# Performance work log

Hardware: AMD Instinct MI355X
Metric: run time of the kernel (lower is better)

The kernel has to match this reference:

```python
import jax, jax.numpy as jnp
import numpy as np

N, NS, IN_P, OUT_P, SHARE = 65536, 16, 256, 256, 8
MID = OUT_P
EPS = 1e-5


def _bn(x, gamma, beta):
    # torch BatchNorm1d (training mode, biased var) applied over the channel
    # (last) axis; stats over all other axes. Matches BN on x.transpose(1,2).
    mean = x.mean(axis=(0, 1), keepdims=True)
    var = ((x - mean) ** 2).mean(axis=(0, 1), keepdims=True)
    return gamma * (x - mean) * jax.lax.rsqrt(var + EPS) + beta


def setup_inputs() -> dict:
    key = jax.random.key(0)
    ks = jax.random.split(key, 12)
    w = lambda k, shape: jax.random.normal(k, shape, dtype=jnp.float32) * 0.02
    return {
        "p": jax.random.uniform(ks[0], (N, 3), dtype=jnp.float32),
        "x": jax.random.normal(ks[1], (N, IN_P), dtype=jnp.float32),
        "idx": jax.random.randint(ks[2], (N, NS), 0, N),
        "wq": w(ks[3], (MID, IN_P)), "bq": jnp.zeros((MID,), jnp.float32),
        "wk": w(ks[4], (MID, IN_P)), "bk": jnp.zeros((MID,), jnp.float32),
        "wv": w(ks[5], (OUT_P, IN_P)), "bv": jnp.zeros((OUT_P,), jnp.float32),
        "wp1": w(ks[6], (3, 3)), "bp1": jnp.zeros((3,), jnp.float32),
        "gp": jnp.ones((3,), jnp.float32), "btp": jnp.zeros((3,), jnp.float32),
        "wp2": w(ks[7], (OUT_P, 3)), "bp2": jnp.zeros((OUT_P,), jnp.float32),
        "g1": jnp.ones((MID,), jnp.float32), "b1": jnp.zeros((MID,), jnp.float32),
        "ww1": w(ks[8], (MID // SHARE, MID)), "bw1": jnp.zeros((MID // SHARE,), jnp.float32),
        "g2": jnp.ones((MID // SHARE,), jnp.float32), "b2": jnp.zeros((MID // SHARE,), jnp.float32),
        "ww2": w(ks[9], (OUT_P // SHARE, OUT_P // SHARE)), "bw2": jnp.zeros((OUT_P // SHARE,), jnp.float32),
    }


def reference(p, x, idx, wq, bq, wk, bk, wv, bv, wp1, bp1, gp, btp, wp2, bp2,
              g1, b1, ww1, bw1, g2, b2, ww2, bw2):
    # q/k/v projections: [N, C]
    xq = x @ wq.T + bq
    xk = x @ wk.T + bk
    xv = x @ wv.T + bv
    # queryandgroup: gather neighbor features + relative positions
    xk_g = xk[idx]                      # [N, NS, MID]
    xv_g = xv[idx]                      # [N, NS, OUT_P]
    p_r = p[idx] - p[:, None, :]        # [N, NS, 3]  (use_xyz relative coords)
    # linear_p: Linear(3,3) -> BN(3) -> ReLU -> Linear(3, OUT_P)
    p_r = p_r @ wp1.T + bp1
    p_r = jax.nn.relu(_bn(p_r, gp, btp))
    p_r = p_r @ wp2.T + bp2             # [N, NS, OUT_P]
    # vector attention logits; out_planes // mid_planes == 1 so the
    # view(...).sum(2) of p_r is just p_r
    w = xk_g - xq[:, None, :] + p_r     # [N, NS, MID]
    # linear_w: BN -> ReLU -> Linear(MID, MID/S) -> BN -> ReLU -> Linear
    w = jax.nn.relu(_bn(w, g1, b1))
    w = w @ ww1.T + bw1                 # [N, NS, MID/S]
    w = jax.nn.relu(_bn(w, g2, b2))
    w = w @ ww2.T + bw2                 # [N, NS, OUT_P/S]
    w = jax.nn.softmax(w, axis=1)       # softmax over neighbors
    # grouped weighted sum with shared attention planes
    n, ns, c = xv_g.shape
    out = ((xv_g + p_r).reshape(n, ns, SHARE, c // SHARE)
           * w[:, :, None, :]).sum(axis=1).reshape(n, c)
    return out
```

## Files before the change

kernel.cpp:

```cpp
#include <hip/hip_runtime.h>
#include <hip/hip_bf16.h>

#define NPTS 65536
#define NSAMP 16
#define CH 256
#define CNT (NPTS * NSAMP)
#define EPSV 1e-5f

typedef __hip_bfloat16 bf16;
typedef __attribute__((ext_vector_type(8))) short short8;
typedef __attribute__((ext_vector_type(4))) short sh4;
typedef __attribute__((ext_vector_type(4))) float floatx4;

__device__ __forceinline__ float b2f(bf16 v) { return __bfloat162float(v); }

__device__ __forceinline__ float s2f(short v) {
    return __uint_as_float(((unsigned)(unsigned short)v) << 16);
}

__device__ __forceinline__ short f2bf_bits(float f) {
    bf16 h = __float2bfloat16(f);
    short s;
    __builtin_memcpy(&s, &h, 2);
    return s;
}

__global__ __launch_bounds__(256) void convw_kernel(
    const float* __restrict__ wq, const float* __restrict__ wk,
    const float* __restrict__ wv, const float* __restrict__ ww2,
    const float* __restrict__ x,
    bf16* __restrict__ Wcat, bf16* __restrict__ ww2b, bf16* __restrict__ xb)
{
    if (blockIdx.x < 96) {
        int e = (blockIdx.x * 256 + threadIdx.x) * 8;
        const float* src = (e < 65536) ? wq : (e < 131072) ? wk : wv;
        int off = e & 65535;
        float4 f0 = *(const float4*)(src + off);
        float4 f1 = *(const float4*)(src + off + 4);
        short8 r;
        r[0] = f2bf_bits(f0.x); r[1] = f2bf_bits(f0.y);
        r[2] = f2bf_bits(f0.z); r[3] = f2bf_bits(f0.w);
        r[4] = f2bf_bits(f1.x); r[5] = f2bf_bits(f1.y);
        r[6] = f2bf_bits(f1.z); r[7] = f2bf_bits(f1.w);
        *(short8*)(Wcat + e) = r;
    } else if (blockIdx.x == 96) {
        int e = threadIdx.x * 4;
        float4 f = *(const float4*)(ww2 + e);
        sh4 r;
        r[0] = f2bf_bits(f.x); r[1] = f2bf_bits(f.y);
        r[2] = f2bf_bits(f.z); r[3] = f2bf_bits(f.w);
        *(sh4*)(ww2b + e) = r;
    } else {
        size_t e = ((size_t)(blockIdx.x - 97) * 256 + threadIdx.x) * 8;
        float4 f0 = *(const float4*)(x + e);
        float4 f1 = *(const float4*)(x + e + 4);
        short8 r;
        r[0] = f2bf_bits(f0.x); r[1] = f2bf_bits(f0.y);
        r[2] = f2bf_bits(f0.z); r[3] = f2bf_bits(f0.w);
        r[4] = f2bf_bits(f1.x); r[5] = f2bf_bits(f1.y);
        r[6] = f2bf_bits(f1.z); r[7] = f2bf_bits(f1.w);
        *(short8*)(xb + e) = r;
    }
}

__global__ __launch_bounds__(256) void gemm_kernel(
    const bf16* __restrict__ xb, const bf16* __restrict__ Wcat,
    const float* __restrict__ bq, const float* __restrict__ bk,
    const float* __restrict__ bv,
    bf16* __restrict__ xq, bf16* __restrict__ xk, bf16* __restrict__ xv)
{
    __shared__ __align__(16) bf16 As[128 * 40];
    __shared__ __align__(16) bf16 Bs[128 * 40];

    int t = threadIdx.x, lane = t & 63, wave = t >> 6;
    int m0 = blockIdx.x * 128;
    int y = blockIdx.y, n0 = y * 128;
    int srow = t >> 1, sch = t & 1;
    int m = lane & 15, q = lane >> 4;
    int wm = wave >> 1, wn = wave & 1;

    floatx4 acc[4][4];
#pragma unroll
    for (int a = 0; a < 4; a++)
#pragma unroll
        for (int b = 0; b < 4; b++) acc[a][b] = (floatx4){0.f, 0.f, 0.f, 0.f};

    for (int kk = 0; kk < 256; kk += 32) {
        const bf16* ap = xb + (size_t)(m0 + srow) * 256 + kk + sch * 16;
        *(short8*)&As[srow * 40 + sch * 16]     = *(const short8*)ap;
        *(short8*)&As[srow * 40 + sch * 16 + 8] = *(const short8*)(ap + 8);
        const bf16* bp = Wcat + (size_t)(n0 + srow) * 256 + kk + sch * 16;
        *(short8*)&Bs[srow * 40 + sch * 16]     = *(const short8*)bp;
        *(short8*)&Bs[srow * 40 + sch * 16 + 8] = *(const short8*)(bp + 8);
        __syncthreads();

        short8 av[4], bvv[4];
#pragma unroll
        for (int mt = 0; mt < 4; mt++)
            av[mt] = *(const short8*)&As[(wm * 64 + mt * 16 + m) * 40 + q * 8];
#pragma unroll
        for (int nt = 0; nt < 4; nt++)
            bvv[nt] = *(const short8*)&Bs[(wn * 64 + nt * 16 + m) * 40 + q * 8];
#pragma unroll
        for (int mt = 0; mt < 4; mt++)
#pragma unroll
            for (int nt = 0; nt < 4; nt++)
                acc[mt][nt] = __builtin_amdgcn_mfma_f32_16x16x32_bf16(av[mt], bvv[nt], acc[mt][nt], 0, 0, 0);
        __syncthreads();
    }

    int z = y >> 1;
    bf16* O        = (z == 0) ? xq : (z == 1) ? xk : xv;
    const float* B = (z == 0) ? bq : (z == 1) ? bk : bv;
    int cbase = (y & 1) * 128 + wn * 64;
#pragma unroll
    for (int nt = 0; nt < 4; nt++) {
        int oc = cbase + nt * 16 + m;
        float bias = B[oc];
#pragma unroll
        for (int mt = 0; mt < 4; mt++) {
            int grow = m0 + wm * 64 + mt * 16 + q * 4;
#pragma unroll
            for (int i = 0; i < 4; i++)
                O[(size_t)(grow + i) * 256 + oc] = __float2bfloat16(acc[mt][nt][i] + bias);
        }
    }
}

__global__ __launch_bounds__(256) void statsp_kernel(
    const float* __restrict__ p, const int* __restrict__ idx,
    const float* __restrict__ wp1, const float* __restrict__ bp1,
    float* __restrict__ statsP, float4* __restrict__ v4)
{
    __shared__ float red[4][6];

    float W00 = wp1[0], W01 = wp1[1], W02 = wp1[2];
    float W10 = wp1[3], W11 = wp1[4], W12 = wp1[5];
    float W20 = wp1[6], W21 = wp1[7], W22 = wp1[8];
    float B0 = bp1[0], B1 = bp1[1], B2 = bp1[2];

    float s0 = 0, s1 = 0, s2 = 0, q0 = 0, q1 = 0, q2 = 0;
    int stride = gridDim.x * blockDim.x;
    for (int r = blockIdx.x * blockDim.x + threadIdx.x; r < CNT; r += stride) {
        int n = r >> 4;
        int i = idx[r];
        float a0 = p[3 * (size_t)i]     - p[3 * (size_t)n];
        float a1 = p[3 * (size_t)i + 1] - p[3 * (size_t)n + 1];
        float a2 = p[3 * (size_t)i + 2] - p[3 * (size_t)n + 2];
        float v0 = W00 * a0 + W01 * a1 + W02 * a2 + B0;
        float v1 = W10 * a0 + W11 * a1 + W12 * a2 + B1;
        float v2 = W20 * a0 + W21 * a1 + W22 * a2 + B2;
        s0 += v0; q0 += v0 * v0;
        s1 += v1; q1 += v1 * v1;
        s2 += v2; q2 += v2 * v2;
        v4[r] = make_float4(v0, v1, v2, 0.f);
    }
    float v[6] = {s0, s1, s2, q0, q1, q2};
    int wave = threadIdx.x >> 6;
#pragma unroll
    for (int k = 0; k < 6; k++) {
        float xv = v[k];
#pragma unroll
        for (int off = 32; off > 0; off >>= 1) xv += __shfl_down(xv, off);
        if ((threadIdx.x & 63) == 0) red[wave][k] = xv;
    }
    __syncthreads();
    if (threadIdx.x < 6) {
        float s = red[0][threadIdx.x] + red[1][threadIdx.x]
                + red[2][threadIdx.x] + red[3][threadIdx.x];
        atomicAdd(&statsP[threadIdx.x * 16], s);
    }
}

__global__ void finalize_kernel(const float* __restrict__ stats,
                                const float* __restrict__ gamma,
                                const float* __restrict__ beta,
                                float* __restrict__ ss, int nch, int sstr)
{
    int c = threadIdx.x;
    if (c < nch) {
        float inv = 1.0f / (float)CNT;
        float mean = stats[c * sstr] * inv;
        float var = stats[(nch + c) * sstr] * inv - mean * mean;
        float sc = gamma[c] * rsqrtf(var + EPSV);
        ss[c] = sc;
        ss[nch + c] = beta[c] - mean * sc;
    }
}

__global__ __launch_bounds__(256) void computer_kernel(
    const float* __restrict__ ssP, float4* __restrict__ r4)
{
    float sc0 = ssP[0], sc1 = ssP[1], sc2 = ssP[2];
    float sh0 = ssP[3], sh1 = ssP[4], sh2 = ssP[5];

    int stride = gridDim.x * blockDim.x;
    for (int r = blockIdx.x * blockDim.x + threadIdx.x; r < CNT; r += stride) {
        float4 v = r4[r];
        float v0 = fmaxf(sc0 * v.x + sh0, 0.f);
        float v1 = fmaxf(sc1 * v.y + sh1, 0.f);
        float v2 = fmaxf(sc2 * v.z + sh2, 0.f);
        r4[r] = make_float4(v0, v1, v2, 0.f);
    }
}

__global__ __launch_bounds__(256) void stats1_kernel(
    const int* __restrict__ idx, const float4* __restrict__ r4,
    const bf16* __restrict__ xk, const bf16* __restrict__ xq,
    const float* __restrict__ wp2, const float* __restrict__ bp2,
    float* __restrict__ stats1)
{
    __shared__ int idxs[1024];
    __shared__ float redS[8 * 264];
    __shared__ float redQ[8 * 264];

    int t = threadIdx.x;
    int r0 = blockIdx.x * 1024;
    for (int e = t; e < 1024; e += 256) idxs[e] = idx[r0 + e];

    int sub = t & 31, rl = t >> 5, cb = sub * 8;
    float w0[8], w1[8], w2[8], bc[8];
#pragma unroll
    for (int k = 0; k < 8; k++) {
        w0[k] = wp2[3 * (cb + k)];
        w1[k] = wp2[3 * (cb + k) + 1];
        w2[k] = wp2[3 * (cb + k) + 2];
        bc[k] = bp2[cb + k];
    }
    float s8[8] = {0, 0, 0, 0, 0, 0, 0, 0};
    float q8[8] = {0, 0, 0, 0, 0, 0, 0, 0};
    __syncthreads();

#pragma unroll 4
    for (int rr = rl; rr < 1024; rr += 8) {
        int r = r0 + rr;
        int i = idxs[rr];
        float4 rv = r4[r];
        short8 kv = *(const short8*)(xk + (size_t)i * 256 + cb);
        short8 qv = *(const short8*)(xq + (size_t)(r >> 4) * 256 + cb);
#pragma unroll
        for (int k = 0; k < 8; k++) {
            float w = s2f(kv[k]) - s2f(qv[k]) + rv.x * w0[k] + rv.y * w1[k] + rv.z * w2[k] + bc[k];
            s8[k] += w; q8[k] += w * w;
        }
    }
#pragma unroll
    for (int k = 0; k < 8; k++) {
        redS[rl * 264 + cb + k] = s8[k];
        redQ[rl * 264 + cb + k] = q8[k];
    }
    __syncthreads();
    int c = t;
    float ts = 0, tq = 0;
#pragma unroll
    for (int sr = 0; sr < 8; sr++) {
        ts += redS[sr * 264 + c];
        tq += redQ[sr * 264 + c];
    }
    atomicAdd(&stats1[c], ts);
    atomicAdd(&stats1[256 + c], tq);
}

__global__ __launch_bounds__(256) void stats2_kernel(
    const int* __restrict__ idx, const float4* __restrict__ r4,
    const bf16* __restrict__ xk, const bf16* __restrict__ xq,
    const float* __restrict__ wp2, const float* __restrict__ bp2,
    const float* __restrict__ ss1,
    const float* __restrict__ ww1, const float* __restrict__ bw1,
    bf16* __restrict__ y2, float* __restrict__ stats2)
{
    __shared__ __align__(16) bf16 hb0[64 * 256];
    __shared__ __align__(16) bf16 hb1[64 * 256];

    int t = threadIdx.x;
    int lane = t & 63, wave = t >> 6;
    int m = lane & 15, q = lane >> 4;
    int sub = t & 31, rl = t >> 5, cb = sub * 8;
    int r0 = blockIdx.x * 1024;

    short8 bf0[8], bf1[8];
#pragma unroll
    for (int k = 0; k < 8; k++) {
        const float* w0p = ww1 + m * 256 + k * 32 + q * 8;
        const float* w1p = ww1 + (16 + m) * 256 + k * 32 + q * 8;
        float4 u0 = *(const float4*)(w0p);
        float4 u1 = *(const float4*)(w0p + 4);
        float4 u2 = *(const float4*)(w1p);
        float4 u3 = *(const float4*)(w1p + 4);
        short8 b0, b1;
        b0[0] = f2bf_bits(u0.x); b0[1] = f2bf_bits(u0.y);
        b0[2] = f2bf_bits(u0.z); b0[3] = f2bf_bits(u0.w);
        b0[4] = f2bf_bits(u1.x); b0[5] = f2bf_bits(u1.y);
        b0[6] = f2bf_bits(u1.z); b0[7] = f2bf_bits(u1.w);
        b1[0] = f2bf_bits(u2.x); b1[1] = f2bf_bits(u2.y);
        b1[2] = f2bf_bits(u2.z); b1[3] = f2bf_bits(u2.w);
        b1[4] = f2bf_bits(u3.x); b1[5] = f2bf_bits(u3.y);
        b1[6] = f2bf_bits(u3.z); b1[7] = f2bf_bits(u3.w);
        bf0[k] = b0; bf1[k] = b1;
    }

    float w0[8], w1[8], w2[8], bc[8], s1c[8], t1c[8];
#pragma unroll
    for (int k = 0; k < 8; k++) {
        w0[k] = wp2[3 * (cb + k)];
        w1[k] = wp2[3 * (cb + k) + 1];
        w2[k] = wp2[3 * (cb + k) + 2];
        bc[k] = bp2[cb + k];
        s1c[k] = ss1[cb + k];
        t1c[k] = ss1[256 + cb + k];
    }
    float bw0 = bw1[m], bw16 = bw1[16 + m];
    float jsum0 = 0, jsum1 = 0, jsq0 = 0, jsq1 = 0;
    int swh = cb ^ (rl << 3);
    int swa = (m & 7) << 3;

    {
#pragma unroll
        for (int u = 0; u < 8; u++) {
            int rr = rl + u * 8;
            int r = r0 + rr;
            int i = idx[r];
            float4 rv = r4[r];
            short8 kv = *(const short8*)(xk + (size_t)i * 256 + cb);
            short8 qv = *(const short8*)(xq + (size_t)(r >> 4) * 256 + cb);
            short8 h;
#pragma unroll
            for (int k = 0; k < 8; k++) {
                float w = s2f(kv[k]) - s2f(qv[k]) + rv.x * w0[k] + rv.y * w1[k] + rv.z * w2[k] + bc[k];
                h[k] = f2bf_bits(fmaxf(s1c[k] * w + t1c[k], 0.f));
            }
            *(short8*)&hb0[rr * 256 + swh] = h;
        }
    }

    for (int it = 0; it < 16; ++it) {
        __syncthreads();

        int rbn = r0 + (it + 1) * 64;
        bf16* hbw = (it & 1) ? hb0 : hb1;
        const bf16* abase = ((it & 1) ? hb1 : hb0) + (wave * 16 + m) * 256;

        short8 kvs[8];
        if (it < 15) {
#pragma unroll
            for (int u = 0; u < 8; u++) {
                int r = rbn + rl + u * 8;
                kvs[u] = *(const short8*)(xk + (size_t)idx[r] * 256 + cb);
            }
        }

        floatx4 a0 = (floatx4){bw0, bw0, bw0, bw0};
        floatx4 a1 = (floatx4){bw16, bw16, bw16, bw16};
#pragma unroll
        for (int k = 0; k < 8; k++) {
            int col = (k * 32 + q * 8) ^ swa;
            short8 af = *(const short8*)(abase + col);
            a0 = __builtin_amdgcn_mfma_f32_16x16x32_bf16(af, bf0[k], a0, 0, 0, 0);
            a1 = __builtin_amdgcn_mfma_f32_16x16x32_bf16(af, bf1[k], a1, 0, 0, 0);
        }
        int grow = r0 + it * 64 + wave * 16 + q * 4;
#pragma unroll
        for (int ii = 0; ii < 4; ii++) {
            float y0 = a0[ii];
            float y1 = a1[ii];
            jsum0 += y0; jsq0 += y0 * y0;
            jsum1 += y1; jsq1 += y1 * y1;
            y2[(size_t)(grow + ii) * 32 + m]      = __float2bfloat16(y0);
            y2[(size_t)(grow + ii) * 32 + 16 + m] = __float2bfloat16(y1);
        }

        if (it < 15) {
#pragma unroll
            for (int u = 0; u < 8; u++) {
                int rr = rl + u * 8;
                int r = rbn + rr;
                float4 rv = r4[r];
                short8 qv = *(const short8*)(xq + (size_t)(r >> 4) * 256 + cb);
                short8 h;
#pragma unroll
                for (int k = 0; k < 8; k++) {
                    float w = s2f(kvs[u][k]) - s2f(qv[k]) + rv.x * w0[k] + rv.y * w1[k] + rv.z * w2[k] + bc[k];
                    h[k] = f2bf_bits(fmaxf(s1c[k] * w + t1c[k], 0.f));
                }
                *(short8*)&hbw[rr * 256 + swh] = h;
            }
        }
    }

    jsum0 += __shfl_xor(jsum0, 16); jsum0 += __shfl_xor(jsum0, 32);
    jsum1 += __shfl_xor(jsum1, 16); jsum1 += __shfl_xor(jsum1, 32);
    jsq0  += __shfl_xor(jsq0, 16);  jsq0  += __shfl_xor(jsq0, 32);
    jsq1  += __shfl_xor(jsq1, 16);  jsq1  += __shfl_xor(jsq1, 32);
    if (q == 0) {
        atomicAdd(&stats2[m], jsum0);
        atomicAdd(&stats2[16 + m], jsum1);
        atomicAdd(&stats2[32 + m], jsq0);
        atomicAdd(&stats2[48 + m], jsq1);
    }
}

__global__ __launch_bounds__(256) void final_kernel(
    const int* __restrict__ idx, const float4* __restrict__ r4,
    const bf16* __restrict__ xv,
    const float* __restrict__ wp2, const float* __restrict__ bp2,
    const bf16* __restrict__ y2, const float* __restrict__ ss2,
    const bf16* __restrict__ ww2b, const float* __restrict__ bw2,
    float* __restrict__ out)
{
    __shared__ __align__(16) float wsm[4][16][36];
    __shared__ float Asm[4][4][32];

    int t = threadIdx.x, wave = t >> 6, lane = t & 63;
    int m = lane & 15, q = lane >> 4;

    short8 bf0 = *(const short8*)(ww2b + m * 32 + q * 8);
    short8 bf1 = *(const short8*)(ww2b + (16 + m) * 32 + q * 8);
    float bwj0 = bw2[m], bwj1 = bw2[16 + m];

    float s2c[8], t2c[8];
#pragma unroll
    for (int k = 0; k < 8; k++) {
        s2c[k] = ss2[q * 8 + k];
        t2c[k] = ss2[32 + q * 8 + k];
    }

    int c0 = lane * 4;
    int j4 = (lane & 7) * 4;
    float wpc0[4], wpc1[4], wpc2[4], bpc[4];
#pragma unroll
    for (int k = 0; k < 4; k++) {
        wpc0[k] = wp2[(c0 + k) * 3];
        wpc1[k] = wp2[(c0 + k) * 3 + 1];
        wpc2[k] = wp2[(c0 + k) * 3 + 2];
        bpc[k]  = bp2[c0 + k];
    }

    int pbase = (blockIdx.x * 4 + wave) * 8;
    for (int pp = 0; pp < 8; pp++) {
        int n = pbase + pp;
        size_t rbase = (size_t)n * 16;

        int iv = idx[rbase + m];

        short8 yv = *(const short8*)(y2 + (rbase + m) * 32 + q * 8);
        short8 av;
#pragma unroll
        for (int k = 0; k < 8; k++)
            av[k] = f2bf_bits(fmaxf(s2c[k] * s2f(yv[k]) + t2c[k], 0.f));

        floatx4 l0 = (floatx4){bwj0, bwj0, bwj0, bwj0};
        floatx4 l1 = (floatx4){bwj1, bwj1, bwj1, bwj1};
        l0 = __builtin_amdgcn_mfma_f32_16x16x32_bf16(av, bf0, l0, 0, 0, 0);
        l1 = __builtin_amdgcn_mfma_f32_16x16x32_bf16(av, bf1, l1, 0, 0, 0);

        float mx0 = fmaxf(fmaxf(l0[0], l0[1]), fmaxf(l0[2], l0[3]));
        float mx1 = fmaxf(fmaxf(l1[0], l1[1]), fmaxf(l1[2], l1[3]));
        mx0 = fmaxf(mx0, __shfl_xor(mx0, 16));
        mx0 = fmaxf(mx0, __shfl_xor(mx0, 32));
        mx1 = fmaxf(mx1, __shfl_xor(mx1, 16));
        mx1 = fmaxf(mx1, __shfl_xor(mx1, 32));
        float w0[4], w1[4];
        float sum0 = 0.f, sum1 = 0.f;
#pragma unroll
        for (int i = 0; i < 4; i++) {
            w0[i] = __expf(l0[i] - mx0); sum0 += w0[i];
            w1[i] = __expf(l1[i] - mx1); sum1 += w1[i];
        }
        sum0 += __shfl_xor(sum0, 16); sum0 += __shfl_xor(sum0, 32);
        sum1 += __shfl_xor(sum1, 16); sum1 += __shfl_xor(sum1, 32);
        float inv0 = 1.f / sum0, inv1 = 1.f / sum1;

        float A00 = 0, A10 = 0, A20 = 0, A30 = 0;
        float A01 = 0, A11 = 0, A21 = 0, A31 = 0;
#pragma unroll
        for (int i = 0; i < 4; i++) {
            w0[i] *= inv0; w1[i] *= inv1;
            float4 rv = r4[rbase + q * 4 + i];
            A00 += rv.x * w0[i]; A10 += rv.y * w0[i];
            A20 += rv.z * w0[i]; A30 += w0[i];
            A01 += rv.x * w1[i]; A11 += rv.y * w1[i];
            A21 += rv.z * w1[i]; A31 += w1[i];
            wsm[wave][q * 4 + i][m]      = w0[i];
            wsm[wave][q * 4 + i][16 + m] = w1[i];
        }
        A00 += __shfl_xor(A00, 16); A00 += __shfl_xor(A00, 32);
        A10 += __shfl_xor(A10, 16); A10 += __shfl_xor(A10, 32);
        A20 += __shfl_xor(A20, 16); A20 += __shfl_xor(A20, 32);
        A30 += __shfl_xor(A30, 16); A30 += __shfl_xor(A30, 32);
        A01 += __shfl_xor(A01, 16); A01 += __shfl_xor(A01, 32);
        A11 += __shfl_xor(A11, 16); A11 += __shfl_xor(A11, 32);
        A21 += __shfl_xor(A21, 16); A21 += __shfl_xor(A21, 32);
        A31 += __shfl_xor(A31, 16); A31 += __shfl_xor(A31, 32);
        if (q == 0) {
            Asm[wave][0][m] = A00; Asm[wave][1][m] = A10;
            Asm[wave][2][m] = A20; Asm[wave][3][m] = A30;
            Asm[wave][0][16 + m] = A01; Asm[wave][1][16 + m] = A11;
            Asm[wave][2][16 + m] = A21; Asm[wave][3][16 + m] = A31;
        }

        float acc0 = 0, acc1 = 0, acc2 = 0, acc3 = 0;
#pragma unroll
        for (int s = 0; s < 16; s++) {
            int i = __builtin_amdgcn_readlane(iv, s);
            sh4 vv = *(const sh4*)(xv + (size_t)i * 256 + c0);
            float4 wv = *(const float4*)&wsm[wave][s][j4];
            acc0 += s2f(vv[0]) * wv.x;
            acc1 += s2f(vv[1]) * wv.y;
            acc2 += s2f(vv[2]) * wv.z;
            acc3 += s2f(vv[3]) * wv.w;
        }

        float res[4] = {acc0, acc1, acc2, acc3};
#pragma unroll
        for (int k = 0; k < 4; k++) {
            int j = j4 + k;
            res[k] += wpc0[k] * Asm[wave][0][j] + wpc1[k] * Asm[wave][1][j]
                    + wpc2[k] * Asm[wave][2][j] + bpc[k]  * Asm[wave][3][j];
        }
        *(float4*)(out + (size_t)n * 256 + c0) =
            make_float4(res[0], res[1], res[2], res[3]);
    }
}

extern "C" void kernel_launch(void* const* d_in, const int* in_sizes, int n_in,
                              void* d_out, int out_size, void* d_ws, size_t ws_size,
                              hipStream_t stream) {
    (void)in_sizes; (void)n_in; (void)out_size; (void)ws_size;

    const float* p   = (const float*)d_in[0];
    const float* x   = (const float*)d_in[1];
    const int*   idx = (const int*)d_in[2];
    const float* wq  = (const float*)d_in[3];  const float* bq  = (const float*)d_in[4];
    const float* wk  = (const float*)d_in[5];  const float* bk  = (const float*)d_in[6];
    const float* wv  = (const float*)d_in[7];  const float* bv  = (const float*)d_in[8];
    const float* wp1 = (const float*)d_in[9];  const float* bp1 = (const float*)d_in[10];
    const float* gp  = (const float*)d_in[11]; const float* btp = (const float*)d_in[12];
    const float* wp2 = (const float*)d_in[13]; const float* bp2 = (const float*)d_in[14];
    const float* g1  = (const float*)d_in[15]; const float* b1  = (const float*)d_in[16];
    const float* ww1 = (const float*)d_in[17]; const float* bw1 = (const float*)d_in[18];
    const float* g2  = (const float*)d_in[19]; const float* b2  = (const float*)d_in[20];
    const float* ww2 = (const float*)d_in[21]; const float* bw2 = (const float*)d_in[22];
    float* out = (float*)d_out;

    float* fws    = (float*)d_ws;
    float* statsP = fws;
    float* ssP    = fws + 96;
    float* stats1 = fws + 112;
    float* ss1    = fws + 624;
    float* stats2 = fws + 1136;
    float* ss2    = fws + 1200;
    bf16* ww2b = (bf16*)((char*)d_ws + 6144);
    bf16* Wcat = (bf16*)((char*)d_ws + 8192);
    bf16* xq = (bf16*)((char*)d_ws + 401408);
    bf16* xk = xq + (size_t)NPTS * CH;
    bf16* xv = xk + (size_t)NPTS * CH;
    bf16* y2 = xv + (size_t)NPTS * CH;
    float4* r4 = (float4*)(y2 + (size_t)CNT * 32);
    bf16* xb = y2;

    hipMemsetAsync(d_ws, 0, 8192, stream);

    convw_kernel<<<97 + 8192, 256, 0, stream>>>(wq, wk, wv, ww2, x, Wcat, ww2b, xb);
    gemm_kernel<<<dim3(512, 6), 256, 0, stream>>>(xb, Wcat, bq, bk, bv, xq, xk, xv);
    statsp_kernel<<<1024, 256, 0, stream>>>(p, idx, wp1, bp1, statsP, r4);
    finalize_kernel<<<1, 256, 0, stream>>>(statsP, gp, btp, ssP, 3, 16);
    computer_kernel<<<1024, 256, 0, stream>>>(ssP, r4);
    stats1_kernel<<<1024, 256, 0, stream>>>(idx, r4, xk, xq, wp2, bp2, stats1);
    finalize_kernel<<<1, 256, 0, stream>>>(stats1, g1, b1, ss1, 256, 1);
    stats2_kernel<<<1024, 256, 0, stream>>>(idx, r4, xk, xq, wp2, bp2, ss1, ww1, bw1, y2, stats2);
    finalize_kernel<<<1, 256, 0, stream>>>(stats2, g2, b2, ss2, 32, 1);
    final_kernel<<<NPTS / 32, 256, 0, stream>>>(idx, r4, xv, wp2, bp2, y2, ss2, ww2b, bw2, out);
}
```

Before: 663.6 us.

## Fuse position-stats into conversion kernel, apply BN-ReLU on load, widen stats2 blocks

The position BN statistics pass now runs inside the weight/x conversion kernel as extra blocks, which saves one launch and lets the two passes overlap. The separate pass that rewrote r4 with BN+ReLU is removed; each consumer kernel applies the scale/shift and ReLU when it loads r4. This drops a full read-write sweep over a 16 MB buffer at the price of a little repeated ALU work. stats2 now uses 512-thread blocks with 8 waves split into 4 row-groups × 2 column halves, so each wave issues one MFMA chain instead of two and fewer gathers per thread. That trades per-wave register use for more parallelism.

```diff
diff --git a/kernel.cpp b/kernel.cpp
--- a/kernel.cpp
+++ b/kernel.cpp
@@ -25,14 +25,56 @@
     return s;
 }
 
-__global__ __launch_bounds__(256) void convw_kernel(
+__global__ __launch_bounds__(256) void fused0_kernel(
     const float* __restrict__ wq, const float* __restrict__ wk,
     const float* __restrict__ wv, const float* __restrict__ ww2,
-    const float* __restrict__ x,
-    bf16* __restrict__ Wcat, bf16* __restrict__ ww2b, bf16* __restrict__ xb)
+    const float* __restrict__ x, const float* __restrict__ p,
+    const int* __restrict__ idx,
+    const float* __restrict__ wp1, const float* __restrict__ bp1,
+    bf16* __restrict__ Wcat, bf16* __restrict__ ww2b, bf16* __restrict__ xb,
+    float* __restrict__ statsP, float4* __restrict__ v4)
 {
-    if (blockIdx.x < 96) {
-        int e = (blockIdx.x * 256 + threadIdx.x) * 8;
+    __shared__ float red[4][6];
+    int bid = blockIdx.x;
+
+    if (bid < 1024) {
+        float W00 = wp1[0], W01 = wp1[1], W02 = wp1[2];
+        float W10 = wp1[3], W11 = wp1[4], W12 = wp1[5];
+        float W20 = wp1[6], W21 = wp1[7], W22 = wp1[8];
+        float B0 = bp1[0], B1 = bp1[1], B2 = bp1[2];
+
+        float s0 = 0, s1 = 0, s2 = 0, q0 = 0, q1 = 0, q2 = 0;
+        for (int r = bid * 256 + threadIdx.x; r < CNT; r += 1024 * 256) {
+            int n = r >> 4;
+            int i = idx[r];
+            float a0 = p[3 * (size_t)i]     - p[3 * (size_t)n];
+            float a1 = p[3 * (size_t)i + 1] - p[3 * (size_t)n + 1];
+            float a2 = p[3 * (size_t)i + 2] - p[3 * (size_t)n + 2];
+            float v0 = W00 * a0 + W01 * a1 + W02 * a2 + B0;
+            float v1 = W10 * a0 + W11 * a1 + W12 * a2 + B1;
+            float v2 = W20 * a0 + W21 * a1 + W22 * a2 + B2;
+            s0 += v0; q0 += v0 * v0;
+            s1 += v1; q1 += v1 * v1;
+            s2 += v2; q2 += v2 * v2;
+            v4[r] = make_float4(v0, v1, v2, 0.f);
+        }
+        float v[6] = {s0, s1, s2, q0, q1, q2};
+        int wave = threadIdx.x >> 6;
+#pragma unroll
+        for (int k = 0; k < 6; k++) {
+            float xv = v[k];
+#pragma unroll
+            for (int off = 32; off > 0; off >>= 1) xv += __shfl_down(xv, off);
+            if ((threadIdx.x & 63) == 0) red[wave][k] = xv;
+        }
+        __syncthreads();
+        if (threadIdx.x < 6) {
+            float s = red[0][threadIdx.x] + red[1][threadIdx.x]
+                    + red[2][threadIdx.x] + red[3][threadIdx.x];
+            atomicAdd(&statsP[threadIdx.x * 16], s);
+        }
+    } else if (bid < 1120) {
+        int e = ((bid - 1024) * 256 + threadIdx.x) * 8;
         const float* src = (e < 65536) ? wq : (e < 131072) ? wk : wv;
         int off = e & 65535;
         float4 f0 = *(const float4*)(src + off);
@@ -43,7 +85,7 @@
         r[4] = f2bf_bits(f1.x); r[5] = f2bf_bits(f1.y);
         r[6] = f2bf_bits(f1.z); r[7] = f2bf_bits(f1.w);
         *(short8*)(Wcat + e) = r;
-    } else if (blockIdx.x == 96) {
+    } else if (bid == 1120) {
         int e = threadIdx.x * 4;
         float4 f = *(const float4*)(ww2 + e);
         sh4 r;
@@ -51,7 +93,7 @@
         r[2] = f2bf_bits(f.z); r[3] = f2bf_bits(f.w);
         *(sh4*)(ww2b + e) = r;
     } else {
-        size_t e = ((size_t)(blockIdx.x - 97) * 256 + threadIdx.x) * 8;
+        size_t e = ((size_t)(bid - 1121) * 256 + threadIdx.x) * 8;
         float4 f0 = *(const float4*)(x + e);
         float4 f1 = *(const float4*)(x + e + 4);
         short8 r;
@@ -124,51 +166,6 @@
             for (int i = 0; i < 4; i++)
                 O[(size_t)(grow + i) * 256 + oc] = __float2bfloat16(acc[mt][nt][i] + bias);
         }
-    }
-}
-
-__global__ __launch_bounds__(256) void statsp_kernel(
-    const float* __restrict__ p, const int* __restrict__ idx,
-    const float* __restrict__ wp1, const float* __restrict__ bp1,
-    float* __restrict__ statsP, float4* __restrict__ v4)
-{
-    __shared__ float red[4][6];
-
-    float W00 = wp1[0], W01 = wp1[1], W02 = wp1[2];
-    float W10 = wp1[3], W11 = wp1[4], W12 = wp1[5];
-    float W20 = wp1[6], W21 = wp1[7], W22 = wp1[8];
-    float B0 = bp1[0], B1 = bp1[1], B2 = bp1[2];
-
-    float s0 = 0, s1 = 0, s2 = 0, q0 = 0, q1 = 0, q2 = 0;
-    int stride = gridDim.x * blockDim.x;
-    for (int r = blockIdx.x * blockDim.x + threadIdx.x; r < CNT; r += stride) {
-        int n = r >> 4;
-        int i = idx[r];
-        float a0 = p[3 * (size_t)i]     - p[3 * (size_t)n];
-        float a1 = p[3 * (size_t)i + 1] - p[3 * (size_t)n + 1];
-        float a2 = p[3 * (size_t)i + 2] - p[3 * (size_t)n + 2];
-        float v0 = W00 * a0 + W01 * a1 + W02 * a2 + B0;
-        float v1 = W10 * a0 + W11 * a1 + W12 * a2 + B1;
-        float v2 = W20 * a0 + W21 * a1 + W22 * a2 + B2;
-        s0 += v0; q0 += v0 * v0;
-        s1 += v1; q1 += v1 * v1;
-        s2 += v2; q2 += v2 * v2;
-        v4[r] = make_float4(v0, v1, v2, 0.f);
-    }
-    float v[6] = {s0, s1, s2, q0, q1, q2};
-    int wave = threadIdx.x >> 6;
-#pragma unroll
-    for (int k = 0; k < 6; k++) {
-        float xv = v[k];
-#pragma unroll
-        for (int off = 32; off > 0; off >>= 1) xv += __shfl_down(xv, off);
-        if ((threadIdx.x & 63) == 0) red[wave][k] = xv;
-    }
-    __syncthreads();
-    if (threadIdx.x < 6) {
-        float s = red[0][threadIdx.x] + red[1][threadIdx.x]
-                + red[2][threadIdx.x] + red[3][threadIdx.x];
-        atomicAdd(&statsP[threadIdx.x * 16], s);
     }
 }
 
@@ -188,27 +185,11 @@
     }
 }
 
-__global__ __launch_bounds__(256) void computer_kernel(
-    const float* __restrict__ ssP, float4* __restrict__ r4)
-{
-    float sc0 = ssP[0], sc1 = ssP[1], sc2 = ssP[2];
-    float sh0 = ssP[3], sh1 = ssP[4], sh2 = ssP[5];
-
-    int stride = gridDim.x * blockDim.x;
-    for (int r = blockIdx.x * blockDim.x + threadIdx.x; r < CNT; r += stride) {
-        float4 v = r4[r];
-        float v0 = fmaxf(sc0 * v.x + sh0, 0.f);
-        float v1 = fmaxf(sc1 * v.y + sh1, 0.f);
-        float v2 = fmaxf(sc2 * v.z + sh2, 0.f);
-        r4[r] = make_float4(v0, v1, v2, 0.f);
-    }
-}
-
 __global__ __launch_bounds__(256) void stats1_kernel(
     const int* __restrict__ idx, const float4* __restrict__ r4,
     const bf16* __restrict__ xk, const bf16* __restrict__ xq,
     const float* __restrict__ wp2, const float* __restrict__ bp2,
-    float* __restrict__ stats1)
+    const float* __restrict__ ssP, float* __restrict__ stats1)
 {
     __shared__ int idxs[1024];
     __shared__ float redS[8 * 264];
@@ -227,6 +208,8 @@
         w2[k] = wp2[3 * (cb + k) + 2];
         bc[k] = bp2[cb + k];
     }
+    float scP0 = ssP[0], scP1 = ssP[1], scP2 = ssP[2];
+    float shP0 = ssP[3], shP1 = ssP[4], shP2 = ssP[5];
     float s8[8] = {0, 0, 0, 0, 0, 0, 0, 0};
     float q8[8] = {0, 0, 0, 0, 0, 0, 0, 0};
     __syncthreads();
@@ -235,12 +218,15 @@
     for (int rr = rl; rr < 1024; rr += 8) {
         int r = r0 + rr;
         int i = idxs[rr];
-        float4 rv = r4[r];
+        float4 va = r4[r];
+        float rx = fmaxf(scP0 * va.x + shP0, 0.f);
+        float ry = fmaxf(scP1 * va.y + shP1, 0.f);
+        float rz = fmaxf(scP2 * va.z + shP2, 0.f);
         short8 kv = *(const short8*)(xk + (size_t)i * 256 + cb);
         short8 qv = *(const short8*)(xq + (size_t)(r >> 4) * 256 + cb);
 #pragma unroll
         for (int k = 0; k < 8; k++) {
-            float w = s2f(kv[k]) - s2f(qv[k]) + rv.x * w0[k] + rv.y * w1[k] + rv.z * w2[k] + bc[k];
+            float w = s2f(kv[k]) - s2f(qv[k]) + rx * w0[k] + ry * w1[k] + rz * w2[k] + bc[k];
             s8[k] += w; q8[k] += w * w;
         }
     }
@@ -261,11 +247,11 @@
     atomicAdd(&stats1[256 + c], tq);
 }
 
-__global__ __launch_bounds__(256) void stats2_kernel(
+__global__ __launch_bounds__(512, 4) void stats2_kernel(
     const int* __restrict__ idx, const float4* __restrict__ r4,
     const bf16* __restrict__ xk, const bf16* __restrict__ xq,
     const float* __restrict__ wp2, const float* __restrict__ bp2,
-    const float* __restrict__ ss1,
+    const float* __restrict__ ssP, const float* __restrict__ ss1,
     const float* __restrict__ ww1, const float* __restrict__ bw1,
     bf16* __restrict__ y2, float* __restrict__ stats2)
 {
@@ -275,28 +261,22 @@
     int t = threadIdx.x;
     int lane = t & 63, wave = t >> 6;
     int m = lane & 15, q = lane >> 4;
+    int wr = wave >> 1, wc = wave & 1;
     int sub = t & 31, rl = t >> 5, cb = sub * 8;
     int r0 = blockIdx.x * 1024;
 
-    short8 bf0[8], bf1[8];
+    short8 bf[8];
 #pragma unroll
     for (int k = 0; k < 8; k++) {
-        const float* w0p = ww1 + m * 256 + k * 32 + q * 8;
-        const float* w1p = ww1 + (16 + m) * 256 + k * 32 + q * 8;
-        float4 u0 = *(const float4*)(w0p);
-        float4 u1 = *(const float4*)(w0p + 4);
-        float4 u2 = *(const float4*)(w1p);
-        float4 u3 = *(const float4*)(w1p + 4);
-        short8 b0, b1;
-        b0[0] = f2bf_bits(u0.x); b0[1] = f2bf_bits(u0.y);
-        b0[2] = f2bf_bits(u0.z); b0[3] = f2bf_bits(u0.w);
-        b0[4] = f2bf_bits(u1.x); b0[5] = f2bf_bits(u1.y);
-        b0[6] = f2bf_bits(u1.z); b0[7] = f2bf_bits(u1.w);
-        b1[0] = f2bf_bits(u2.x); b1[1] = f2bf_bits(u2.y);
-        b1[2] = f2bf_bits(u2.z); b1[3] = f2bf_bits(u2.w);
-        b1[4] = f2bf_bits(u3.x); b1[5] = f2bf_bits(u3.y);
-        b1[6] = f2bf_bits(u3.z); b1[7] = f2bf_bits(u3.w);
-        bf0[k] = b0; bf1[k] = b1;
+        const float* wp = ww1 + (wc * 16 + m) * 256 + k * 32 + q * 8;
+        float4 u0 = *(const float4*)(wp);
+        float4 u1 = *(const float4*)(wp + 4);
+        short8 b;
+        b[0] = f2bf_bits(u0.x); b[1] = f2bf_bits(u0.y);
+        b[2] = f2bf_bits(u0.z); b[3] = f2bf_bits(u0.w);
+        b[4] = f2bf_bits(u1.x); b[5] = f2bf_bits(u1.y);
+        b[6] = f2bf_bits(u1.z); b[7] = f2bf_bits(u1.w);
+        bf[k] = b;
     }
 
     float w0[8], w1[8], w2[8], bc[8], s1c[8], t1c[8];
@@ -309,28 +289,31 @@
         s1c[k] = ss1[cb + k];
         t1c[k] = ss1[256 + cb + k];
     }
-    float bw0 = bw1[m], bw16 = bw1[16 + m];
-    float jsum0 = 0, jsum1 = 0, jsq0 = 0, jsq1 = 0;
-    int swh = cb ^ (rl << 3);
+    float scP0 = ssP[0], scP1 = ssP[1], scP2 = ssP[2];
+    float shP0 = ssP[3], shP1 = ssP[4], shP2 = ssP[5];
+    float bwv = bw1[wc * 16 + m];
+    float jsum = 0, jsq = 0;
+    int swh = cb ^ ((rl & 7) << 3);
     int swa = (m & 7) << 3;
 
-    {
-#pragma unroll
-        for (int u = 0; u < 8; u++) {
-            int rr = rl + u * 8;
-            int r = r0 + rr;
-            int i = idx[r];
-            float4 rv = r4[r];
-            short8 kv = *(const short8*)(xk + (size_t)i * 256 + cb);
-            short8 qv = *(const short8*)(xq + (size_t)(r >> 4) * 256 + cb);
-            short8 h;
-#pragma unroll
-            for (int k = 0; k < 8; k++) {
-                float w = s2f(kv[k]) - s2f(qv[k]) + rv.x * w0[k] + rv.y * w1[k] + rv.z * w2[k] + bc[k];
-                h[k] = f2bf_bits(fmaxf(s1c[k] * w + t1c[k], 0.f));
-            }
-            *(short8*)&hb0[rr * 256 + swh] = h;
-        }
+#pragma unroll
+    for (int u = 0; u < 4; u++) {
+        int rr = rl + u * 16;
+        int r = r0 + rr;
+        int i = idx[r];
+        float4 va = r4[r];
+        float rx = fmaxf(scP0 * va.x + shP0, 0.f);
+        float ry = fmaxf(scP1 * va.y + shP1, 0.f);
+        float rz = fmaxf(scP2 * va.z + shP2, 0.f);
+        short8 kv = *(const short8*)(xk + (size_t)i * 256 + cb);
+        short8 qv = *(const short8*)(xq + (size_t)(r >> 4) * 256 + cb);
+        short8 h;
+#pragma unroll
+        for (int k = 0; k < 8; k++) {
+            float w = s2f(kv[k]) - s2f(qv[k]) + rx * w0[k] + ry * w1[k] + rz * w2[k] + bc[k];
+            h[k] = f2bf_bits(fmaxf(s1c[k] * w + t1c[k], 0.f));
+        }
+        *(short8*)&hb0[rr * 256 + swh] = h;
     }
 
     for (int it = 0; it < 16; ++it) {
@@ -338,48 +321,46 @@
 
         int rbn = r0 + (it + 1) * 64;
         bf16* hbw = (it & 1) ? hb0 : hb1;
-        const bf16* abase = ((it & 1) ? hb1 : hb0) + (wave * 16 + m) * 256;
-
-        short8 kvs[8];
+        const bf16* abase = ((it & 1) ? hb1 : hb0) + (wr * 16 + m) * 256;
+
+        short8 kvs[4];
         if (it < 15) {
 #pragma unroll
-            for (int u = 0; u < 8; u++) {
-                int r = rbn + rl + u * 8;
+            for (int u = 0; u < 4; u++) {
+                int r = rbn + rl + u * 16;
                 kvs[u] = *(const short8*)(xk + (size_t)idx[r] * 256 + cb);
             }
         }
 
-        floatx4 a0 = (floatx4){bw0, bw0, bw0, bw0};
-        floatx4 a1 = (floatx4){bw16, bw16, bw16, bw16};
+        floatx4 a = (floatx4){bwv, bwv, bwv, bwv};
 #pragma unroll
         for (int k = 0; k < 8; k++) {
             int col = (k * 32 + q * 8) ^ swa;
             short8 af = *(const short8*)(abase + col);
-            a0 = __builtin_amdgcn_mfma_f32_16x16x32_bf16(af, bf0[k], a0, 0, 0, 0);
-            a1 = __builtin_amdgcn_mfma_f32_16x16x32_bf16(af, bf1[k], a1, 0, 0, 0);
-        }
-        int grow = r0 + it * 64 + wave * 16 + q * 4;
+            a = __builtin_amdgcn_mfma_f32_16x16x32_bf16(af, bf[k], a, 0, 0, 0);
+        }
+        int grow = r0 + it * 64 + wr * 16 + q * 4;
 #pragma unroll
         for (int ii = 0; ii < 4; ii++) {
-            float y0 = a0[ii];
-            float y1 = a1[ii];
-            jsum0 += y0; jsq0 += y0 * y0;
-            jsum1 += y1; jsq1 += y1 * y1;
-            y2[(size_t)(grow + ii) * 32 + m]      = __float2bfloat16(y0);
-            y2[(size_t)(grow + ii) * 32 + 16 + m] = __float2bfloat16(y1);
+            float y = a[ii];
+            jsum += y; jsq += y * y;
+            y2[(size_t)(grow + ii) * 32 + wc * 16 + m] = __float2bfloat16(y);
         }
 
         if (it < 15) {
 #pragma unroll
-            for (int u = 0; u < 8; u++) {
-                int rr = rl + u * 8;
+            for (int u = 0; u < 4; u++) {
+                int rr = rl + u * 16;
                 int r = rbn + rr;
-                float4 rv = r4[r];
+                float4 va = r4[r];
+                float rx = fmaxf(scP0 * va.x + shP0, 0.f);
+                float ry = fmaxf(scP1 * va.y + shP1, 0.f);
+                float rz = fmaxf(scP2 * va.z + shP2, 0.f);
                 short8 qv = *(const short8*)(xq + (size_t)(r >> 4) * 256 + cb);
                 short8 h;
 #pragma unroll
                 for (int k = 0; k < 8; k++) {
-                    float w = s2f(kvs[u][k]) - s2f(qv[k]) + rv.x * w0[k] + rv.y * w1[k] + rv.z * w2[k] + bc[k];
+                    float w = s2f(kvs[u][k]) - s2f(qv[k]) + rx * w0[k] + ry * w1[k] + rz * w2[k] + bc[k];
                     h[k] = f2bf_bits(fmaxf(s1c[k] * w + t1c[k], 0.f));
                 }
                 *(short8*)&hbw[rr * 256 + swh] = h;
@@ -387,15 +368,11 @@
         }
     }
 
-    jsum0 += __shfl_xor(jsum0, 16); jsum0 += __shfl_xor(jsum0, 32);
-    jsum1 += __shfl_xor(jsum1, 16); jsum1 += __shfl_xor(jsum1, 32);
-    jsq0  += __shfl_xor(jsq0, 16);  jsq0  += __shfl_xor(jsq0, 32);
-    jsq1  += __shfl_xor(jsq1, 16);  jsq1  += __shfl_xor(jsq1, 32);
+    jsum += __shfl_xor(jsum, 16); jsum += __shfl_xor(jsum, 32);
+    jsq  += __shfl_xor(jsq, 16);  jsq  += __shfl_xor(jsq, 32);
     if (q == 0) {
-        atomicAdd(&stats2[m], jsum0);
-        atomicAdd(&stats2[16 + m], jsum1);
-        atomicAdd(&stats2[32 + m], jsq0);
-        atomicAdd(&stats2[48 + m], jsq1);
+        atomicAdd(&stats2[wc * 16 + m], jsum);
+        atomicAdd(&stats2[32 + wc * 16 + m], jsq);
     }
 }
 
@@ -405,7 +382,7 @@
     const float* __restrict__ wp2, const float* __restrict__ bp2,
     const bf16* __restrict__ y2, const float* __restrict__ ss2,
     const bf16* __restrict__ ww2b, const float* __restrict__ bw2,
-    float* __restrict__ out)
+    const float* __restrict__ ssP, float* __restrict__ out)
 {
     __shared__ __align__(16) float wsm[4][16][36];
     __shared__ float Asm[4][4][32];
@@ -423,6 +400,8 @@
         s2c[k] = ss2[q * 8 + k];
         t2c[k] = ss2[32 + q * 8 + k];
     }
+    float scP0 = ssP[0], scP1 = ssP[1], scP2 = ssP[2];
+    float shP0 = ssP[3], shP1 = ssP[4], shP2 = ssP[5];
 
     int c0 = lane * 4;
     int j4 = (lane & 7) * 4;
@@ -475,11 +454,14 @@
 #pragma unroll
         for (int i = 0; i < 4; i++) {
             w0[i] *= inv0; w1[i] *= inv1;
-            float4 rv = r4[rbase + q * 4 + i];
-            A00 += rv.x * w0[i]; A10 += rv.y * w0[i];
-            A20 += rv.z * w0[i]; A30 += w0[i];
-            A01 += rv.x * w1[i]; A11 += rv.y * w1[i];
-            A21 += rv.z * w1[i]; A31 += w1[i];
+            float4 va = r4[rbase + q * 4 + i];
+            float rx = fmaxf(scP0 * va.x + shP0, 0.f);
+            float ry = fmaxf(scP1 * va.y + shP1, 0.f);
+            float rz = fmaxf(scP2 * va.z + shP2, 0.f);
+            A00 += rx * w0[i]; A10 += ry * w0[i];
+            A20 += rz * w0[i]; A30 += w0[i];
+            A01 += rx * w1[i]; A11 += ry * w1[i];
+            A21 += rz * w1[i]; A31 += w1[i];
             wsm[wave][q * 4 + i][m]      = w0[i];
             wsm[wave][q * 4 + i][16 + m] = w1[i];
         }
@@ -560,14 +542,13 @@
 
     hipMemsetAsync(d_ws, 0, 8192, stream);
 
-    convw_kernel<<<97 + 8192, 256, 0, stream>>>(wq, wk, wv, ww2, x, Wcat, ww2b, xb);
+    fused0_kernel<<<1024 + 97 + 8192, 256, 0, stream>>>(
+        wq, wk, wv, ww2, x, p, idx, wp1, bp1, Wcat, ww2b, xb, statsP, r4);
     gemm_kernel<<<dim3(512, 6), 256, 0, stream>>>(xb, Wcat, bq, bk, bv, xq, xk, xv);
-    statsp_kernel<<<1024, 256, 0, stream>>>(p, idx, wp1, bp1, statsP, r4);
     finalize_kernel<<<1, 256, 0, stream>>>(statsP, gp, btp, ssP, 3, 16);
-    computer_kernel<<<1024, 256, 0, stream>>>(ssP, r4);
-    stats1_kernel<<<1024, 256, 0, stream>>>(idx, r4, xk, xq, wp2, bp2, stats1);
+    stats1_kernel<<<1024, 256, 0, stream>>>(idx, r4, xk, xq, wp2, bp2, ssP, stats1);
     finalize_kernel<<<1, 256, 0, stream>>>(stats1, g1, b1, ss1, 256, 1);
-    stats2_kernel<<<1024, 256, 0, stream>>>(idx, r4, xk, xq, wp2, bp2, ss1, ww1, bw1, y2, stats2);
+    stats2_kernel<<<1024, 512, 0, stream>>>(idx, r4, xk, xq, wp2, bp2, ssP, ss1, ww1, bw1, y2, stats2);
     finalize_kernel<<<1, 256, 0, stream>>>(stats2, g2, b2, ss2, 32, 1);
-    final_kernel<<<NPTS / 32, 256, 0, stream>>>(idx, r4, xv, wp2, bp2, y2, ss2, ww2b, bw2, out);
-}
+    final_kernel<<<NPTS / 32, 256, 0, stream>>>(idx, r4, xv, wp2, bp2, y2, ss2, ww2b, bw2, ssP, out);
+}
```

Result: slower. 775.5 us (+16.9%).
